# Optimization experiments

Measured on AMD Instinct MI355X. Metric: run time of the kernel, lower is better.

The kernel has to match this reference:

```python
import jax, jax.numpy as jnp
import numpy as np

N_E, E_DIM, N = 1024, 128, 262144


def setup_inputs() -> dict:
    key = jax.random.key(0)
    kx, kw = jax.random.split(key)
    x = jax.random.normal(kx, (N, E_DIM), dtype=jnp.float32)
    # nn.Embedding weight initialized uniform(-1/n_e, 1/n_e)
    W = jax.random.uniform(kw, (N_E, E_DIM), dtype=jnp.float32,
                           minval=-1.0 / N_E, maxval=1.0 / N_E)
    return {"x": x, "W": W}


def reference(x, W):
    # d[n, k] = ||x_n||^2 + ||W_k||^2 - 2 x_n . W_k   -> shape [N, n_e]
    d = (jnp.sum(x * x, axis=1, keepdims=True)
         + jnp.sum(W * W, axis=1)
         - 2.0 * jnp.matmul(x, W.T))
    min_indices = jnp.argmin(d, axis=1)          # [N] int
    z_q = jnp.take(W, min_indices, axis=0)       # [N, e_dim] gather
    return (z_q, min_indices)
```

## Files before the change

kernel.cpp:

```cpp
#include <hip/hip_runtime.h>

#define EDIM 128
#define NE   1024
#define TAU  7e-5f
#define CAPP 65536

typedef short v8s __attribute__((ext_vector_type(8)));
typedef float v4f __attribute__((ext_vector_type(4)));
typedef __attribute__((address_space(3))) void       lds_t;
typedef const __attribute__((address_space(1))) void gm_t;

__device__ inline unsigned bf16_rne(float f) {
    unsigned u = __float_as_uint(f);
    return (u + 0x7fffu + ((u >> 16) & 1u)) >> 16;
}
__device__ inline float bf16_tof(unsigned h) { return __uint_as_float(h << 16); }

__global__ void vq_prep(const float* __restrict__ W,
                        unsigned short* __restrict__ whiF,
                        unsigned short* __restrict__ wloF,
                        float* __restrict__ Wt,
                        float* __restrict__ swsq_ws)
{
#pragma clang fp contract(off)
    const int t = blockIdx.x * 256 + threadIdx.x;
    #pragma unroll
    for (int rep = 0; rep < 2; ++rep) {
        int o = t + rep * 65536;
        int sub = o >> 11, r = o & 2047;
        int ks = r >> 9, l = (r >> 3) & 63, e = r & 7;
        int src = (sub * 16 + (l & 15)) * EDIM + ks * 32 + (l >> 4) * 8 + e;
        float v = W[src];
        unsigned h = bf16_rne(v);
        whiF[o] = (unsigned short)h;
        wloF[o] = (unsigned short)bf16_rne(v - bf16_tof(h));
        Wt[o] = W[(o & 1023) * EDIM + (o >> 10)];
    }
    if (t < NE) {
        const float4* wr = reinterpret_cast<const float4*>(W) + (size_t)t * 32;
        float4 A = wr[0], B = wr[1];
        float r0 = A.x*A.x, r1 = A.y*A.y, r2 = A.z*A.z, r3 = A.w*A.w;
        float r4 = B.x*B.x, r5 = B.y*B.y, r6 = B.z*B.z, r7 = B.w*B.w;
        #pragma unroll
        for (int i = 2; i < 32; i += 2) {
            float4 C = wr[i], D = wr[i + 1];
            r0 += C.x*C.x; r1 += C.y*C.y; r2 += C.z*C.z; r3 += C.w*C.w;
            r4 += D.x*D.x; r5 += D.y*D.y; r6 += D.z*D.z; r7 += D.w*D.w;
        }
        swsq_ws[t] = ((r0 + r1) + (r2 + r3)) + ((r4 + r5) + (r6 + r7));
    }
}

union SMem {
    struct { unsigned short ring[3][2][4096]; float snwk2h[NE]; } p1;
    struct { float4 scan[2048]; int sbest[128]; } p2;
};

__global__ __launch_bounds__(256, 3) void vq_mfma9(
    const float* __restrict__ x,
    const unsigned short* __restrict__ whiF, const unsigned short* __restrict__ wloF,
    const float* __restrict__ W, const float* __restrict__ swsq_ws,
    float* __restrict__ zq, float* __restrict__ idxout,
    int* __restrict__ cnt_pair, int* __restrict__ cnt_full,
    int* __restrict__ plist, int* __restrict__ flist)
{
    __shared__ SMem sm;

    const int tid = threadIdx.x;
    const int wid = tid >> 6;
    const int l   = tid & 63;
    const int m   = l & 15;
    const int g   = l >> 4;

    const long long row0 = (long long)blockIdx.x * 128;
    const float4* x4 = reinterpret_cast<const float4*>(x);
    const float4* W4 = reinterpret_cast<const float4*>(W);

#define STAGE_TILE(T, B) do {                                                          \
    __builtin_amdgcn_global_load_lds((gm_t*)(whiF + (size_t)(T) * 4096 + tid * 8),     \
        (lds_t*)&sm.p1.ring[B][0][tid * 8], 16, 0, 0);                                 \
    __builtin_amdgcn_global_load_lds((gm_t*)(whiF + (size_t)(T) * 4096 + 2048 + tid * 8), \
        (lds_t*)&sm.p1.ring[B][0][2048 + tid * 8], 16, 0, 0);                          \
    __builtin_amdgcn_global_load_lds((gm_t*)(wloF + (size_t)(T) * 4096 + tid * 8),     \
        (lds_t*)&sm.p1.ring[B][1][tid * 8], 16, 0, 0);                                 \
    __builtin_amdgcn_global_load_lds((gm_t*)(wloF + (size_t)(T) * 4096 + 2048 + tid * 8), \
        (lds_t*)&sm.p1.ring[B][1][2048 + tid * 8], 16, 0, 0);                          \
} while (0)

    STAGE_TILE(0, 0);
    STAGE_TILE(1, 1);

    {
        float4 v = reinterpret_cast<const float4*>(swsq_ws)[tid];
        v.x *= -0.5f; v.y *= -0.5f; v.z *= -0.5f; v.w *= -0.5f;
        reinterpret_cast<float4*>(sm.p1.snwk2h)[tid] = v;
    }

    const long long rA0 = row0 + wid * 32 + m;
    const long long rA1 = rA0 + 16;
    v8s a0h[4], a0l[4], a1h[4], a1l[4];
    #pragma unroll
    for (int ks = 0; ks < 4; ++ks) {
        float4 p0 = x4[rA0 * 32 + ks * 8 + g * 2];
        float4 p1 = x4[rA0 * 32 + ks * 8 + g * 2 + 1];
        float4 q0 = x4[rA1 * 32 + ks * 8 + g * 2];
        float4 q1 = x4[rA1 * 32 + ks * 8 + g * 2 + 1];
        float vp[8] = {p0.x,p0.y,p0.z,p0.w,p1.x,p1.y,p1.z,p1.w};
        float vq[8] = {q0.x,q0.y,q0.z,q0.w,q1.x,q1.y,q1.z,q1.w};
        #pragma unroll
        for (int e = 0; e < 8; ++e) {
            unsigned h0 = bf16_rne(vp[e]);
            a0h[ks][e] = (short)h0;
            a0l[ks][e] = (short)bf16_rne(vp[e] - bf16_tof(h0));
            unsigned h1 = bf16_rne(vq[e]);
            a1h[ks][e] = (short)h1;
            a1l[ks][e] = (short)bf16_rne(vq[e] - bf16_tof(h1));
        }
    }
    __syncthreads();

    float best[8], sec[8]; int bk[8];
    #pragma unroll
    for (int r = 0; r < 8; ++r) { best[r] = -3.4e38f; sec[r] = -3.4e38f; bk[r] = 0; }

    int bcur = 0;
    #pragma unroll 1
    for (int t = 0; t < 32; ++t) {
        if (t + 1 < 32) asm volatile("s_waitcnt vmcnt(4)" ::: "memory");
        else            asm volatile("s_waitcnt vmcnt(0)" ::: "memory");
        __builtin_amdgcn_s_barrier();

        if (t + 2 < 32) {
            int bnext = bcur + 2; if (bnext >= 3) bnext -= 3;
            STAGE_TILE(t + 2, bnext);
        }

        const unsigned short* bh_base = &sm.p1.ring[bcur][0][l * 8];
        const unsigned short* bl_base = &sm.p1.ring[bcur][1][l * 8];

        #pragma unroll
        for (int half = 0; half < 2; ++half) {
            const int k = t * 32 + half * 16 + m;
            const int hb = half * 2048;
            v8s bh0 = *(const v8s*)(bh_base + hb);
            v8s bh1 = *(const v8s*)(bh_base + hb + 512);
            v8s bh2 = *(const v8s*)(bh_base + hb + 1024);
            v8s bh3 = *(const v8s*)(bh_base + hb + 1536);
            v8s bl0 = *(const v8s*)(bl_base + hb);
            v8s bl1 = *(const v8s*)(bl_base + hb + 512);
            v8s bl2 = *(const v8s*)(bl_base + hb + 1024);
            v8s bl3 = *(const v8s*)(bl_base + hb + 1536);

            const float h = sm.p1.snwk2h[k];
            v4f acc0 = {h, h, h, h};
            v4f acc1 = {h, h, h, h};
            __builtin_amdgcn_s_setprio(1);
            acc0 = __builtin_amdgcn_mfma_f32_16x16x32_bf16(a0h[0], bh0, acc0, 0, 0, 0);
            acc0 = __builtin_amdgcn_mfma_f32_16x16x32_bf16(a0l[0], bh0, acc0, 0, 0, 0);
            acc0 = __builtin_amdgcn_mfma_f32_16x16x32_bf16(a0h[0], bl0, acc0, 0, 0, 0);
            acc1 = __builtin_amdgcn_mfma_f32_16x16x32_bf16(a1h[0], bh0, acc1, 0, 0, 0);
            acc1 = __builtin_amdgcn_mfma_f32_16x16x32_bf16(a1l[0], bh0, acc1, 0, 0, 0);
            acc1 = __builtin_amdgcn_mfma_f32_16x16x32_bf16(a1h[0], bl0, acc1, 0, 0, 0);
            acc0 = __builtin_amdgcn_mfma_f32_16x16x32_bf16(a0h[1], bh1, acc0, 0, 0, 0);
            acc0 = __builtin_amdgcn_mfma_f32_16x16x32_bf16(a0l[1], bh1, acc0, 0, 0, 0);
            acc0 = __builtin_amdgcn_mfma_f32_16x16x32_bf16(a0h[1], bl1, acc0, 0, 0, 0);
            acc1 = __builtin_amdgcn_mfma_f32_16x16x32_bf16(a1h[1], bh1, acc1, 0, 0, 0);
            acc1 = __builtin_amdgcn_mfma_f32_16x16x32_bf16(a1l[1], bh1, acc1, 0, 0, 0);
            acc1 = __builtin_amdgcn_mfma_f32_16x16x32_bf16(a1h[1], bl1, acc1, 0, 0, 0);
            acc0 = __builtin_amdgcn_mfma_f32_16x16x32_bf16(a0h[2], bh2, acc0, 0, 0, 0);
            acc0 = __builtin_amdgcn_mfma_f32_16x16x32_bf16(a0l[2], bh2, acc0, 0, 0, 0);
            acc0 = __builtin_amdgcn_mfma_f32_16x16x32_bf16(a0h[2], bl2, acc0, 0, 0, 0);
            acc1 = __builtin_amdgcn_mfma_f32_16x16x32_bf16(a1h[2], bh2, acc1, 0, 0, 0);
            acc1 = __builtin_amdgcn_mfma_f32_16x16x32_bf16(a1l[2], bh2, acc1, 0, 0, 0);
            acc1 = __builtin_amdgcn_mfma_f32_16x16x32_bf16(a1h[2], bl2, acc1, 0, 0, 0);
            acc0 = __builtin_amdgcn_mfma_f32_16x16x32_bf16(a0h[3], bh3, acc0, 0, 0, 0);
            acc0 = __builtin_amdgcn_mfma_f32_16x16x32_bf16(a0l[3], bh3, acc0, 0, 0, 0);
            acc0 = __builtin_amdgcn_mfma_f32_16x16x32_bf16(a0h[3], bl3, acc0, 0, 0, 0);
            acc1 = __builtin_amdgcn_mfma_f32_16x16x32_bf16(a1h[3], bh3, acc1, 0, 0, 0);
            acc1 = __builtin_amdgcn_mfma_f32_16x16x32_bf16(a1l[3], bh3, acc1, 0, 0, 0);
            acc1 = __builtin_amdgcn_mfma_f32_16x16x32_bf16(a1h[3], bl3, acc1, 0, 0, 0);
            __builtin_amdgcn_s_setprio(0);

            #pragma unroll
            for (int r = 0; r < 4; ++r) {
                float b0 = best[r];
                float a0r = acc0[r];
                sec[r]  = __builtin_amdgcn_fmed3f(a0r, b0, sec[r]);
                bk[r]   = (a0r > b0) ? k : bk[r];
                best[r] = fmaxf(b0, a0r);
                float b1 = best[4 + r];
                float a1r = acc1[r];
                sec[4+r]  = __builtin_amdgcn_fmed3f(a1r, b1, sec[4+r]);
                bk[4+r]   = (a1r > b1) ? k : bk[4+r];
                best[4+r] = fmaxf(b1, a1r);
            }
        }

        bcur = (bcur == 2) ? 0 : bcur + 1;
    }
    __syncthreads();

    #pragma unroll
    for (int r = 0; r < 8; ++r) {
        int rowL = wid * 32 + ((r >> 2) << 4) + (g << 2) + (r & 3);
        float4 e;
        e.x = -2.f * best[r]; e.y = -2.f * sec[r];
        e.z = __int_as_float(bk[r]); e.w = 0.f;
        sm.p2.scan[rowL * 16 + m] = e;
    }
    __syncthreads();

    if (tid < 128) {
        const int stag = tid & 7;
        float b1 = 3.4e38f; int k1 = 0x7fffffff;
        #pragma unroll 1
        for (int mm = 0; mm < 16; ++mm) {
            float4 e = sm.p2.scan[tid * 16 + (mm ^ stag)];
            int kk = __float_as_int(e.z);
            if (e.x < b1 || (e.x == b1 && kk < k1)) { b1 = e.x; k1 = kk; }
        }
        const float th = b1 + TAU;
        int nb = 0; bool asec = false;
        float b2 = 3.4e38f; int k2 = 0x7fffffff;
        #pragma unroll 1
        for (int mm = 0; mm < 16; ++mm) {
            float4 e = sm.p2.scan[tid * 16 + (mm ^ stag)];
            int kk = __float_as_int(e.z);
            nb  += (e.x <= th) ? 1 : 0;
            asec = asec || (e.y <= th);
            if (kk != k1 && (e.x < b2 || (e.x == b2 && kk < k2))) { b2 = e.x; k2 = kk; }
        }
        sm.p2.sbest[tid] = k1;
        idxout[row0 + tid] = (float)k1;
        const int row = (int)(row0 + tid);
        if (asec || nb > 2) {
            int s2 = atomicAdd(cnt_full, 1);
            flist[s2] = row;
        } else if (nb == 2) {
            int slot = atomicAdd(cnt_pair, 1);
            if (slot < CAPP) { plist[2 * slot] = row; plist[2 * slot + 1] = k2; }
            else { int s2 = atomicAdd(cnt_full, 1); flist[s2] = row; }
        }
    }
    __syncthreads();

    float4* zq4 = reinterpret_cast<float4*>(zq);
    for (int i = tid; i < 128 * 32; i += 256) {
        int r = i >> 5, c4 = i & 31;
        zq4[row0 * 32 + i] = W4[(size_t)sm.p2.sbest[r] * 32 + c4];
    }
#undef STAGE_TILE
}

__global__ __launch_bounds__(256, 8) void vq_pair5(
    const float* __restrict__ x, const float* __restrict__ W,
    const float* __restrict__ swsq_ws,
    float* __restrict__ zq, float* __restrict__ idxout,
    const int* __restrict__ cnt_pair, const int* __restrict__ plist)
{
#pragma clang fp contract(off)
    int n = *cnt_pair; if (n > CAPP) n = CAPP;
    const int gsz = gridDim.x * 256;
    for (int i = blockIdx.x * 256 + threadIdx.x; i < n; i += gsz) {
        const int row = plist[2 * i];
        const int k2  = plist[2 * i + 1];
        const int k1  = (int)idxout[row];
        const float4* xr4 = reinterpret_cast<const float4*>(x + (size_t)row * EDIM);
        float4 A = xr4[0], B = xr4[1];
        float r0 = A.x*A.x, r1 = A.y*A.y, r2 = A.z*A.z, r3 = A.w*A.w;
        float r4 = B.x*B.x, r5 = B.y*B.y, r6 = B.z*B.z, r7 = B.w*B.w;
        #pragma unroll
        for (int q = 2; q < 32; q += 2) {
            float4 C = xr4[q], D = xr4[q + 1];
            r0 += C.x*C.x; r1 += C.y*C.y; r2 += C.z*C.z; r3 += C.w*C.w;
            r4 += D.x*D.x; r5 += D.y*D.y; r6 += D.z*D.z; r7 += D.w*D.w;
        }
        float xxv = ((r0 + r1) + (r2 + r3)) + ((r4 + r5) + (r6 + r7));
        const float* xr = x + (size_t)row * EDIM;
        const float* w1 = W + (size_t)k1 * EDIM;
        const float* w2 = W + (size_t)k2 * EDIM;
        float dot1 = 0.f, dot2 = 0.f;
        #pragma unroll 4
        for (int j = 0; j < EDIM; ++j) {
            float a = xr[j];
            dot1 = fmaf(a, w1[j], dot1);
            dot2 = fmaf(a, w2[j], dot2);
        }
        float d1 = (xxv + swsq_ws[k1]) - (dot1 + dot1);
        float d2 = (xxv + swsq_ws[k2]) - (dot2 + dot2);
        int kw = (d2 < d1 || (d2 == d1 && k2 < k1)) ? k2 : k1;
        if (kw != k1) {
            idxout[row] = (float)kw;
            const float4* wr = reinterpret_cast<const float4*>(W) + (size_t)kw * 32;
            float4* zr = reinterpret_cast<float4*>(zq) + (size_t)row * 32;
            #pragma unroll
            for (int q = 0; q < 32; ++q) zr[q] = wr[q];
        }
    }
}

__global__ __launch_bounds__(256, 4) void vq_full5(
    const float* __restrict__ x, const float* __restrict__ Wt,
    const float* __restrict__ W, const float* __restrict__ swsq_ws,
    float* __restrict__ zq, float* __restrict__ idxout,
    const int* __restrict__ cnt_full, const int* __restrict__ flist)
{
#pragma clang fp contract(off)
    const int nf = *cnt_full;
    const int lane = threadIdx.x & 63;
    const int nw = gridDim.x * 4;
    const float4* Wt4 = reinterpret_cast<const float4*>(Wt);
    const float4* W4  = reinterpret_cast<const float4*>(W);
    float4* zq4 = reinterpret_cast<float4*>(zq);

    for (int i = blockIdx.x * 4 + (threadIdx.x >> 6); i < nf; i += nw) {
        const long long row = flist[i];
        const float4* xr4 = reinterpret_cast<const float4*>(x + row * EDIM);
        float xxv;
        {
            float4 A = xr4[0], B = xr4[1];
            float r0 = A.x*A.x, r1 = A.y*A.y, r2 = A.z*A.z, r3 = A.w*A.w;
            float r4 = B.x*B.x, r5 = B.y*B.y, r6 = B.z*B.z, r7 = B.w*B.w;
            #pragma unroll
            for (int q = 2; q < 32; q += 2) {
                float4 C = xr4[q], D = xr4[q + 1];
                r0 += C.x*C.x; r1 += C.y*C.y; r2 += C.z*C.z; r3 += C.w*C.w;
                r4 += D.x*D.x; r5 += D.y*D.y; r6 += D.z*D.z; r7 += D.w*D.w;
            }
            xxv = ((r0 + r1) + (r2 + r3)) + ((r4 + r5) + (r6 + r7));
        }
        float acc[4][4];
        #pragma unroll
        for (int c = 0; c < 4; ++c)
            #pragma unroll
            for (int e = 0; e < 4; ++e) acc[c][e] = 0.f;
        const float* xr = x + row * EDIM;
        #pragma unroll 4
        for (int j = 0; j < EDIM; ++j) {
            float a = xr[j];
            #pragma unroll
            for (int c = 0; c < 4; ++c) {
                float4 w = Wt4[(size_t)j * 256 + c * 64 + lane];
                acc[c][0] = fmaf(a, w.x, acc[c][0]);
                acc[c][1] = fmaf(a, w.y, acc[c][1]);
                acc[c][2] = fmaf(a, w.z, acc[c][2]);
                acc[c][3] = fmaf(a, w.w, acc[c][3]);
            }
        }
        float dbest = 3.4e38f; int bkk = 0;
        #pragma unroll
        for (int c = 0; c < 4; ++c)
            #pragma unroll
            for (int e = 0; e < 4; ++e) {
                int k = c * 256 + lane * 4 + e;
                float t1 = xxv + swsq_ws[k];
                float d  = t1 - (acc[c][e] + acc[c][e]);
                if (d < dbest) { dbest = d; bkk = k; }
            }
        #pragma unroll
        for (int mk = 1; mk < 64; mk <<= 1) {
            float od = __shfl_xor(dbest, mk);
            int   ok = __shfl_xor(bkk, mk);
            if (od < dbest || (od == dbest && ok < bkk)) { dbest = od; bkk = ok; }
        }
        if (lane == 0) idxout[row] = (float)bkk;
        if (lane < 32) zq4[row * 32 + lane] = W4[(size_t)bkk * 32 + lane];
    }
}

__global__ __launch_bounds__(64, 2) void vq_v4(
    const float* __restrict__ x, const float* __restrict__ W,
    float* __restrict__ zq, float* __restrict__ idxout)
{
#pragma clang fp contract(off)
    __shared__ float swsq[NE];
    __shared__ int   sbest[64];
    const int tid = threadIdx.x;
    const long long row0 = (long long)blockIdx.x * 64;
    const long long row  = row0 + tid;
    const float4* x4 = reinterpret_cast<const float4*>(x);
    const float4* W4 = reinterpret_cast<const float4*>(W);
    float4 xr[32];
    #pragma unroll
    for (int i = 0; i < 32; ++i) xr[i] = x4[row * 32 + i];
    #pragma unroll
    for (int i = 0; i < 32; ++i)
        asm volatile("" : "+v"(xr[i].x), "+v"(xr[i].y), "+v"(xr[i].z), "+v"(xr[i].w));
    for (int k = tid; k < NE; k += 64) {
        const float4* wr = W4 + (size_t)k * 32;
        float4 A = wr[0], B = wr[1];
        float r0 = A.x*A.x, r1 = A.y*A.y, r2 = A.z*A.z, r3 = A.w*A.w;
        float r4 = B.x*B.x, r5 = B.y*B.y, r6 = B.z*B.z, r7 = B.w*B.w;
        #pragma unroll
        for (int i = 2; i < 32; i += 2) {
            float4 C = wr[i], D = wr[i + 1];
            r0 += C.x*C.x; r1 += C.y*C.y; r2 += C.z*C.z; r3 += C.w*C.w;
            r4 += D.x*D.x; r5 += D.y*D.y; r6 += D.z*D.z; r7 += D.w*D.w;
        }
        swsq[k] = ((r0 + r1) + (r2 + r3)) + ((r4 + r5) + (r6 + r7));
    }
    float xxv;
    {
        float r0 = xr[0].x*xr[0].x, r1 = xr[0].y*xr[0].y;
        float r2 = xr[0].z*xr[0].z, r3 = xr[0].w*xr[0].w;
        float r4 = xr[1].x*xr[1].x, r5 = xr[1].y*xr[1].y;
        float r6 = xr[1].z*xr[1].z, r7 = xr[1].w*xr[1].w;
        #pragma unroll
        for (int i = 2; i < 32; i += 2) {
            r0 += xr[i].x*xr[i].x;     r1 += xr[i].y*xr[i].y;
            r2 += xr[i].z*xr[i].z;     r3 += xr[i].w*xr[i].w;
            r4 += xr[i+1].x*xr[i+1].x; r5 += xr[i+1].y*xr[i+1].y;
            r6 += xr[i+1].z*xr[i+1].z; r7 += xr[i+1].w*xr[i+1].w;
        }
        xxv = ((r0 + r1) + (r2 + r3)) + ((r4 + r5) + (r6 + r7));
    }
    __syncthreads();
    float dbest = 3.4e38f; int bestk = 0;
    #pragma unroll 1
    for (int k0 = 0; k0 < NE; k0 += 8) {
        float acc[8];
        #pragma unroll
        for (int c = 0; c < 8; ++c) acc[c] = 0.f;
        #pragma unroll
        for (int j4 = 0; j4 < 32; ++j4) {
            const float4 a = xr[j4];
            #pragma unroll
            for (int c = 0; c < 8; ++c) {
                float4 w = W4[(size_t)(k0 + c) * 32 + j4];
                acc[c] = fmaf(a.x, w.x, acc[c]); acc[c] = fmaf(a.y, w.y, acc[c]);
                acc[c] = fmaf(a.z, w.z, acc[c]); acc[c] = fmaf(a.w, w.w, acc[c]);
            }
        }
        #pragma unroll
        for (int c = 0; c < 8; ++c) {
            float t1 = xxv + swsq[k0 + c];
            float d  = t1 - (acc[c] + acc[c]);
            if (d < dbest) { dbest = d; bestk = k0 + c; }
        }
    }
    sbest[tid] = bestk;
    idxout[row] = (float)bestk;
    __syncthreads();
    float4* zq4 = reinterpret_cast<float4*>(zq);
    for (int i = tid; i < 64 * 32; i += 64) {
        int r = i >> 5, c4 = i & 31;
        zq4[row0 * 32 + i] = W4[(size_t)sbest[r] * 32 + c4];
    }
}

extern "C" void kernel_launch(void* const* d_in, const int* in_sizes, int n_in,
                              void* d_out, int out_size, void* d_ws, size_t ws_size,
                              hipStream_t stream) {
    (void)n_in; (void)out_size;
    const float* x = (const float*)d_in[0];
    const float* W = (const float*)d_in[1];
    const int Nrows = in_sizes[0] / EDIM;

    float* zqp    = (float*)d_out;
    float* idxout = zqp + (size_t)Nrows * EDIM;

    const size_t need = 16 + 2 * (size_t)NE * EDIM * 2 + NE * 4
                      + (size_t)NE * EDIM * 4 + (size_t)CAPP * 2 * 4
                      + (size_t)Nrows * 4;
    if (ws_size < need) {
        vq_v4<<<dim3(Nrows / 64), dim3(64), 0, stream>>>(x, W, zqp, idxout);
        return;
    }

    char* p = (char*)d_ws;
    int*            cnt_pair = (int*)p;
    int*            cnt_full = (int*)(p + 4);
    unsigned short* whiF  = (unsigned short*)(p + 16);
    unsigned short* wloF  = whiF + NE * EDIM;
    float*          swsqw = (float*)(wloF + NE * EDIM);
    float*          Wt    = swsqw + NE;
    int*            plist = (int*)(Wt + NE * EDIM);
    int*            flist = plist + CAPP * 2;

    hipMemsetAsync(d_ws, 0, 16, stream);
    vq_prep<<<dim3(256), dim3(256), 0, stream>>>(W, whiF, wloF, Wt, swsqw);
    vq_mfma9<<<dim3(Nrows / 128), dim3(256), 0, stream>>>(x, whiF, wloF, W, swsqw,
                                                          zqp, idxout,
                                                          cnt_pair, cnt_full,
                                                          plist, flist);
    vq_pair5<<<dim3(256), dim3(256), 0, stream>>>(x, W, swsqw, zqp, idxout,
                                                  cnt_pair, plist);
    vq_full5<<<dim3(512), dim3(256), 0, stream>>>(x, Wt, W, swsqw, zqp, idxout,
                                                  cnt_full, flist);
}
```

Baseline: 362.2 us.

## Software-pipeline MFMA tiles with top-2 scan of previous tile

Restructures the main codebook loop into a two-stage software pipeline with two accumulator sets. The MFMA work for tile t is issued before the top-2/argmax update for tile t-1, so the VALU comparison work can overlap the matrix-core latency instead of waiting on freshly produced accumulators. This costs 16 more accumulator registers per lane under a 3-waves launch bound, which raises the risk of spills or lower occupancy.

After: 719.8 us. +98.7%, slower.

```diff
diff --git a/kernel.cpp b/kernel.cpp
--- a/kernel.cpp
+++ b/kernel.cpp
@@ -56,7 +56,9 @@
     struct { float4 scan[2048]; int sbest[128]; } p2;
 };
 
-__global__ __launch_bounds__(256, 3) void vq_mfma9(
+#define MOD3ADD2(v) ((v) >= 1 ? (v) - 1 : 2)
+
+__global__ __launch_bounds__(256, 3) void vq_mfma10(
     const float* __restrict__ x,
     const unsigned short* __restrict__ whiF, const unsigned short* __restrict__ wloF,
     const float* __restrict__ W, const float* __restrict__ swsq_ws,
@@ -85,6 +87,103 @@
         (lds_t*)&sm.p1.ring[B][1][tid * 8], 16, 0, 0);                                 \
     __builtin_amdgcn_global_load_lds((gm_t*)(wloF + (size_t)(T) * 4096 + 2048 + tid * 8), \
         (lds_t*)&sm.p1.ring[B][1][2048 + tid * 8], 16, 0, 0);                          \
+} while (0)
+
+#define WAIT_STAGE(T, BN) do {                                                         \
+    if ((T) + 1 < 32) asm volatile("s_waitcnt vmcnt(4)" ::: "memory");                 \
+    else              asm volatile("s_waitcnt vmcnt(0)" ::: "memory");                 \
+    __builtin_amdgcn_s_barrier();                                                      \
+    if ((T) + 2 < 32) STAGE_TILE((T) + 2, (BN));                                       \
+} while (0)
+
+#define MFMA_TILE(A00, A10, A01, A11, T, B) do {                                       \
+    const unsigned short* bhb = &sm.p1.ring[B][0][l * 8];                              \
+    const unsigned short* blb = &sm.p1.ring[B][1][l * 8];                              \
+    {   const float h = sm.p1.snwk2h[(T) * 32 + m];                                    \
+        A00 = (v4f){h, h, h, h}; A10 = (v4f){h, h, h, h};                              \
+        v8s b0 = *(const v8s*)(bhb);        v8s b1 = *(const v8s*)(bhb + 512);         \
+        v8s b2 = *(const v8s*)(bhb + 1024); v8s b3 = *(const v8s*)(bhb + 1536);        \
+        v8s c0 = *(const v8s*)(blb);        v8s c1 = *(const v8s*)(blb + 512);         \
+        v8s c2 = *(const v8s*)(blb + 1024); v8s c3 = *(const v8s*)(blb + 1536);        \
+        __builtin_amdgcn_s_setprio(1);                                                 \
+        A00 = __builtin_amdgcn_mfma_f32_16x16x32_bf16(a0h[0], b0, A00, 0, 0, 0);       \
+        A00 = __builtin_amdgcn_mfma_f32_16x16x32_bf16(a0l[0], b0, A00, 0, 0, 0);       \
+        A00 = __builtin_amdgcn_mfma_f32_16x16x32_bf16(a0h[0], c0, A00, 0, 0, 0);       \
+        A10 = __builtin_amdgcn_mfma_f32_16x16x32_bf16(a1h[0], b0, A10, 0, 0, 0);       \
+        A10 = __builtin_amdgcn_mfma_f32_16x16x32_bf16(a1l[0], b0, A10, 0, 0, 0);       \
+        A10 = __builtin_amdgcn_mfma_f32_16x16x32_bf16(a1h[0], c0, A10, 0, 0, 0);       \
+        A00 = __builtin_amdgcn_mfma_f32_16x16x32_bf16(a0h[1], b1, A00, 0, 0, 0);       \
+        A00 = __builtin_amdgcn_mfma_f32_16x16x32_bf16(a0l[1], b1, A00, 0, 0, 0);       \
+        A00 = __builtin_amdgcn_mfma_f32_16x16x32_bf16(a0h[1], c1, A00, 0, 0, 0);       \
+        A10 = __builtin_amdgcn_mfma_f32_16x16x32_bf16(a1h[1], b1, A10, 0, 0, 0);       \
+        A10 = __builtin_amdgcn_mfma_f32_16x16x32_bf16(a1l[1], b1, A10, 0, 0, 0);       \
+        A10 = __builtin_amdgcn_mfma_f32_16x16x32_bf16(a1h[1], c1, A10, 0, 0, 0);       \
+        A00 = __builtin_amdgcn_mfma_f32_16x16x32_bf16(a0h[2], b2, A00, 0, 0, 0);       \
+        A00 = __builtin_amdgcn_mfma_f32_16x16x32_bf16(a0l[2], b2, A00, 0, 0, 0);       \
+        A00 = __builtin_amdgcn_mfma_f32_16x16x32_bf16(a0h[2], c2, A00, 0, 0, 0);       \
+        A10 = __builtin_amdgcn_mfma_f32_16x16x32_bf16(a1h[2], b2, A10, 0, 0, 0);       \
+        A10 = __builtin_amdgcn_mfma_f32_16x16x32_bf16(a1l[2], b2, A10, 0, 0, 0);       \
+        A10 = __builtin_amdgcn_mfma_f32_16x16x32_bf16(a1h[2], c2, A10, 0, 0, 0);       \
+        A00 = __builtin_amdgcn_mfma_f32_16x16x32_bf16(a0h[3], b3, A00, 0, 0, 0);       \
+        A00 = __builtin_amdgcn_mfma_f32_16x16x32_bf16(a0l[3], b3, A00, 0, 0, 0);       \
+        A00 = __builtin_amdgcn_mfma_f32_16x16x32_bf16(a0h[3], c3, A00, 0, 0, 0);       \
+        A10 = __builtin_amdgcn_mfma_f32_16x16x32_bf16(a1h[3], b3, A10, 0, 0, 0);       \
+        A10 = __builtin_amdgcn_mfma_f32_16x16x32_bf16(a1l[3], b3, A10, 0, 0, 0);       \
+        A10 = __builtin_amdgcn_mfma_f32_16x16x32_bf16(a1h[3], c3, A10, 0, 0, 0);       \
+        __builtin_amdgcn_s_setprio(0);                                                 \
+    }                                                                                  \
+    {   const float h = sm.p1.snwk2h[(T) * 32 + 16 + m];                               \
+        A01 = (v4f){h, h, h, h}; A11 = (v4f){h, h, h, h};                              \
+        v8s b0 = *(const v8s*)(bhb + 2048); v8s b1 = *(const v8s*)(bhb + 2560);        \
+        v8s b2 = *(const v8s*)(bhb + 3072); v8s b3 = *(const v8s*)(bhb + 3584);        \
+        v8s c0 = *(const v8s*)(blb + 2048); v8s c1 = *(const v8s*)(blb + 2560);        \
+        v8s c2 = *(const v8s*)(blb + 3072); v8s c3 = *(const v8s*)(blb + 3584);        \
+        __builtin_amdgcn_s_setprio(1);                                                 \
+        A01 = __builtin_amdgcn_mfma_f32_16x16x32_bf16(a0h[0], b0, A01, 0, 0, 0);       \
+        A01 = __builtin_amdgcn_mfma_f32_16x16x32_bf16(a0l[0], b0, A01, 0, 0, 0);       \
+        A01 = __builtin_amdgcn_mfma_f32_16x16x32_bf16(a0h[0], c0, A01, 0, 0, 0);       \
+        A11 = __builtin_amdgcn_mfma_f32_16x16x32_bf16(a1h[0], b0, A11, 0, 0, 0);       \
+        A11 = __builtin_amdgcn_mfma_f32_16x16x32_bf16(a1l[0], b0, A11, 0, 0, 0);       \
+        A11 = __builtin_amdgcn_mfma_f32_16x16x32_bf16(a1h[0], c0, A11, 0, 0, 0);       \
+        A01 = __builtin_amdgcn_mfma_f32_16x16x32_bf16(a0h[1], b1, A01, 0, 0, 0);       \
+        A01 = __builtin_amdgcn_mfma_f32_16x16x32_bf16(a0l[1], b1, A01, 0, 0, 0);       \
+        A01 = __builtin_amdgcn_mfma_f32_16x16x32_bf16(a0h[1], c1, A01, 0, 0, 0);       \
+        A11 = __builtin_amdgcn_mfma_f32_16x16x32_bf16(a1h[1], b1, A11, 0, 0, 0);       \
+        A11 = __builtin_amdgcn_mfma_f32_16x16x32_bf16(a1l[1], b1, A11, 0, 0, 0);       \
+        A11 = __builtin_amdgcn_mfma_f32_16x16x32_bf16(a1h[1], c1, A11, 0, 0, 0);       \
+        A01 = __builtin_amdgcn_mfma_f32_16x16x32_bf16(a0h[2], b2, A01, 0, 0, 0);       \
+        A01 = __builtin_amdgcn_mfma_f32_16x16x32_bf16(a0l[2], b2, A01, 0, 0, 0);       \
+        A01 = __builtin_amdgcn_mfma_f32_16x16x32_bf16(a0h[2], c2, A01, 0, 0, 0);       \
+        A11 = __builtin_amdgcn_mfma_f32_16x16x32_bf16(a1h[2], b2, A11, 0, 0, 0);       \
+        A11 = __builtin_amdgcn_mfma_f32_16x16x32_bf16(a1l[2], b2, A11, 0, 0, 0);       \
+        A11 = __builtin_amdgcn_mfma_f32_16x16x32_bf16(a1h[2], c2, A11, 0, 0, 0);       \
+        A01 = __builtin_amdgcn_mfma_f32_16x16x32_bf16(a0h[3], b3, A01, 0, 0, 0);       \
+        A01 = __builtin_amdgcn_mfma_f32_16x16x32_bf16(a0l[3], b3, A01, 0, 0, 0);       \
+        A01 = __builtin_amdgcn_mfma_f32_16x16x32_bf16(a0h[3], c3, A01, 0, 0, 0);       \
+        A11 = __builtin_amdgcn_mfma_f32_16x16x32_bf16(a1h[3], b3, A11, 0, 0, 0);       \
+        A11 = __builtin_amdgcn_mfma_f32_16x16x32_bf16(a1l[3], b3, A11, 0, 0, 0);       \
+        A11 = __builtin_amdgcn_mfma_f32_16x16x32_bf16(a1h[3], c3, A11, 0, 0, 0);       \
+        __builtin_amdgcn_s_setprio(0);                                                 \
+    }                                                                                  \
+} while (0)
+
+#define TOP2_CELL(ACC, R, BI, K) do {                                                  \
+    float b_ = best[BI]; float a_ = ACC[R];                                            \
+    sec[BI]  = __builtin_amdgcn_fmed3f(a_, b_, sec[BI]);                               \
+    bk[BI]   = (a_ > b_) ? (K) : bk[BI];                                               \
+    best[BI] = fmaxf(b_, a_);                                                          \
+} while (0)
+
+#define TOP2_TILE(A00, A10, A01, A11, KB) do {                                         \
+    const int k0_ = (KB) + m; const int k1_ = (KB) + 16 + m;                           \
+    TOP2_CELL(A00, 0, 0, k0_); TOP2_CELL(A00, 1, 1, k0_);                              \
+    TOP2_CELL(A00, 2, 2, k0_); TOP2_CELL(A00, 3, 3, k0_);                              \
+    TOP2_CELL(A10, 0, 4, k0_); TOP2_CELL(A10, 1, 5, k0_);                              \
+    TOP2_CELL(A10, 2, 6, k0_); TOP2_CELL(A10, 3, 7, k0_);                              \
+    TOP2_CELL(A01, 0, 0, k1_); TOP2_CELL(A01, 1, 1, k1_);                              \
+    TOP2_CELL(A01, 2, 2, k1_); TOP2_CELL(A01, 3, 3, k1_);                              \
+    TOP2_CELL(A11, 0, 4, k1_); TOP2_CELL(A11, 1, 5, k1_);                              \
+    TOP2_CELL(A11, 2, 6, k1_); TOP2_CELL(A11, 3, 7, k1_);                              \
 } while (0)
 
     STAGE_TILE(0, 0);
@@ -123,80 +222,29 @@
     #pragma unroll
     for (int r = 0; r < 8; ++r) { best[r] = -3.4e38f; sec[r] = -3.4e38f; bk[r] = 0; }
 
-    int bcur = 0;
+    v4f aA00, aA10, aA01, aA11;
+    v4f aB00, aB10, aB01, aB11;
+
+    WAIT_STAGE(0, 2);
+    MFMA_TILE(aA00, aA10, aA01, aA11, 0, 0);
+
+    int bO = 1, bE = 2;
     #pragma unroll 1
-    for (int t = 0; t < 32; ++t) {
-        if (t + 1 < 32) asm volatile("s_waitcnt vmcnt(4)" ::: "memory");
-        else            asm volatile("s_waitcnt vmcnt(0)" ::: "memory");
-        __builtin_amdgcn_s_barrier();
-
-        if (t + 2 < 32) {
-            int bnext = bcur + 2; if (bnext >= 3) bnext -= 3;
-            STAGE_TILE(t + 2, bnext);
-        }
-
-        const unsigned short* bh_base = &sm.p1.ring[bcur][0][l * 8];
-        const unsigned short* bl_base = &sm.p1.ring[bcur][1][l * 8];
-
-        #pragma unroll
-        for (int half = 0; half < 2; ++half) {
-            const int k = t * 32 + half * 16 + m;
-            const int hb = half * 2048;
-            v8s bh0 = *(const v8s*)(bh_base + hb);
-            v8s bh1 = *(const v8s*)(bh_base + hb + 512);
-            v8s bh2 = *(const v8s*)(bh_base + hb + 1024);
-            v8s bh3 = *(const v8s*)(bh_base + hb + 1536);
-            v8s bl0 = *(const v8s*)(bl_base + hb);
-            v8s bl1 = *(const v8s*)(bl_base + hb + 512);
-            v8s bl2 = *(const v8s*)(bl_base + hb + 1024);
-            v8s bl3 = *(const v8s*)(bl_base + hb + 1536);
-
-            const float h = sm.p1.snwk2h[k];
-            v4f acc0 = {h, h, h, h};
-            v4f acc1 = {h, h, h, h};
-            __builtin_amdgcn_s_setprio(1);
-            acc0 = __builtin_amdgcn_mfma_f32_16x16x32_bf16(a0h[0], bh0, acc0, 0, 0, 0);
-            acc0 = __builtin_amdgcn_mfma_f32_16x16x32_bf16(a0l[0], bh0, acc0, 0, 0, 0);
-            acc0 = __builtin_amdgcn_mfma_f32_16x16x32_bf16(a0h[0], bl0, acc0, 0, 0, 0);
-            acc1 = __builtin_amdgcn_mfma_f32_16x16x32_bf16(a1h[0], bh0, acc1, 0, 0, 0);
-            acc1 = __builtin_amdgcn_mfma_f32_16x16x32_bf16(a1l[0], bh0, acc1, 0, 0, 0);
-            acc1 = __builtin_amdgcn_mfma_f32_16x16x32_bf16(a1h[0], bl0, acc1, 0, 0, 0);
-            acc0 = __builtin_amdgcn_mfma_f32_16x16x32_bf16(a0h[1], bh1, acc0, 0, 0, 0);
-            acc0 = __builtin_amdgcn_mfma_f32_16x16x32_bf16(a0l[1], bh1, acc0, 0, 0, 0);
-            acc0 = __builtin_amdgcn_mfma_f32_16x16x32_bf16(a0h[1], bl1, acc0, 0, 0, 0);
-            acc1 = __builtin_amdgcn_mfma_f32_16x16x32_bf16(a1h[1], bh1, acc1, 0, 0, 0);
-            acc1 = __builtin_amdgcn_mfma_f32_16x16x32_bf16(a1l[1], bh1, acc1, 0, 0, 0);
-            acc1 = __builtin_amdgcn_mfma_f32_16x16x32_bf16(a1h[1], bl1, acc1, 0, 0, 0);
-            acc0 = __builtin_amdgcn_mfma_f32_16x16x32_bf16(a0h[2], bh2, acc0, 0, 0, 0);
-            acc0 = __builtin_amdgcn_mfma_f32_16x16x32_bf16(a0l[2], bh2, acc0, 0, 0, 0);
-            acc0 = __builtin_amdgcn_mfma_f32_16x16x32_bf16(a0h[2], bl2, acc0, 0, 0, 0);
-            acc1 = __builtin_amdgcn_mfma_f32_16x16x32_bf16(a1h[2], bh2, acc1, 0, 0, 0);
-            acc1 = __builtin_amdgcn_mfma_f32_16x16x32_bf16(a1l[2], bh2, acc1, 0, 0, 0);
-            acc1 = __builtin_amdgcn_mfma_f32_16x16x32_bf16(a1h[2], bl2, acc1, 0, 0, 0);
-            acc0 = __builtin_amdgcn_mfma_f32_16x16x32_bf16(a0h[3], bh3, acc0, 0, 0, 0);
-            acc0 = __builtin_amdgcn_mfma_f32_16x16x32_bf16(a0l[3], bh3, acc0, 0, 0, 0);
-            acc0 = __builtin_amdgcn_mfma_f32_16x16x32_bf16(a0h[3], bl3, acc0, 0, 0, 0);
-            acc1 = __builtin_amdgcn_mfma_f32_16x16x32_bf16(a1h[3], bh3, acc1, 0, 0, 0);
-            acc1 = __builtin_amdgcn_mfma_f32_16x16x32_bf16(a1l[3], bh3, acc1, 0, 0, 0);
-            acc1 = __builtin_amdgcn_mfma_f32_16x16x32_bf16(a1h[3], bl3, acc1, 0, 0, 0);
-            __builtin_amdgcn_s_setprio(0);
-
-            #pragma unroll
-            for (int r = 0; r < 4; ++r) {
-                float b0 = best[r];
-                float a0r = acc0[r];
-                sec[r]  = __builtin_amdgcn_fmed3f(a0r, b0, sec[r]);
-                bk[r]   = (a0r > b0) ? k : bk[r];
-                best[r] = fmaxf(b0, a0r);
-                float b1 = best[4 + r];
-                float a1r = acc1[r];
-                sec[4+r]  = __builtin_amdgcn_fmed3f(a1r, b1, sec[4+r]);
-                bk[4+r]   = (a1r > b1) ? k : bk[4+r];
-                best[4+r] = fmaxf(b1, a1r);
-            }
-        }
-
-        bcur = (bcur == 2) ? 0 : bcur + 1;
+    for (int tp = 0; tp < 16; ++tp) {
+        const int tO = 2 * tp + 1;
+        WAIT_STAGE(tO, MOD3ADD2(bO));
+        MFMA_TILE(aB00, aB10, aB01, aB11, tO, bO);
+        TOP2_TILE(aA00, aA10, aA01, aA11, (tO - 1) * 32);
+
+        const int tE = 2 * tp + 2;
+        if (tE < 32) {
+            WAIT_STAGE(tE, MOD3ADD2(bE));
+            MFMA_TILE(aA00, aA10, aA01, aA11, tE, bE);
+        }
+        TOP2_TILE(aB00, aB10, aB01, aB11, tO * 32);
+
+        bO = MOD3ADD2(bO);
+        bE = MOD3ADD2(bE);
     }
     __syncthreads();
 
@@ -250,6 +298,10 @@
         zq4[row0 * 32 + i] = W4[(size_t)sm.p2.sbest[r] * 32 + c4];
     }
 #undef STAGE_TILE
+#undef WAIT_STAGE
+#undef MFMA_TILE
+#undef TOP2_CELL
+#undef TOP2_TILE
 }
 
 __global__ __launch_bounds__(256, 8) void vq_pair5(
@@ -479,10 +531,10 @@
 
     hipMemsetAsync(d_ws, 0, 16, stream);
     vq_prep<<<dim3(256), dim3(256), 0, stream>>>(W, whiF, wloF, Wt, swsqw);
-    vq_mfma9<<<dim3(Nrows / 128), dim3(256), 0, stream>>>(x, whiF, wloF, W, swsqw,
-                                                          zqp, idxout,
-                                                          cnt_pair, cnt_full,
-                                                          plist, flist);
+    vq_mfma10<<<dim3(Nrows / 128), dim3(256), 0, stream>>>(x, whiF, wloF, W, swsqw,
+                                                           zqp, idxout,
+                                                           cnt_pair, cnt_full,
+                                                           plist, flist);
     vq_pair5<<<dim3(256), dim3(256), 0, stream>>>(x, W, swsqw, zqp, idxout,
                                                   cnt_pair, plist);
     vq_full5<<<dim3(512), dim3(256), 0, stream>>>(x, Wt, W, swsqw, zqp, idxout,
```

## Merge pair and full fixup kernels, tighten tolerance, coalesce prep reads

Applied to the files above, without the earlier changes.

Fuses the pair-recheck and full-recompute fixup kernels into one launch with a larger grid, removing one kernel launch and its tail. It also lowers the near-tie tolerance TAU so fewer rows are flagged for exact rechecking, which risks missing true argmin flips. The prep kernel now reads W contiguously and scatters into the MFMA layout instead of gathering. The fused kernel runs the pair phase then the full phase per block with no grid sync, which is safe only if pair and full rows never overlap.

Result: faster. 330.9 us (median of 2 runs) (-8.6%).

```diff
diff --git a/kernel.cpp b/kernel.cpp
--- a/kernel.cpp
+++ b/kernel.cpp
@@ -2,7 +2,7 @@
 
 #define EDIM 128
 #define NE   1024
-#define TAU  7e-5f
+#define TAU  5e-5f
 #define CAPP 65536
 
 typedef short v8s __attribute__((ext_vector_type(8)));
@@ -26,15 +26,17 @@
     const int t = blockIdx.x * 256 + threadIdx.x;
     #pragma unroll
     for (int rep = 0; rep < 2; ++rep) {
-        int o = t + rep * 65536;
-        int sub = o >> 11, r = o & 2047;
-        int ks = r >> 9, l = (r >> 3) & 63, e = r & 7;
-        int src = (sub * 16 + (l & 15)) * EDIM + ks * 32 + (l >> 4) * 8 + e;
-        float v = W[src];
+        int i = t + rep * 65536;
+        float v = W[i];
+        int code = i >> 7, k = i & 127;
+        int sub = code >> 4, m = code & 15;
+        int ks = k >> 5, g = (k >> 3) & 3, e = k & 7;
+        int o = sub * 2048 + ks * 512 + (g * 16 + m) * 8 + e;
         unsigned h = bf16_rne(v);
         whiF[o] = (unsigned short)h;
         wloF[o] = (unsigned short)bf16_rne(v - bf16_tof(h));
-        Wt[o] = W[(o & 1023) * EDIM + (o >> 10)];
+        int o2 = t + rep * 65536;
+        Wt[o2] = W[(o2 & 1023) * EDIM + (o2 >> 10)];
     }
     if (t < NE) {
         const float4* wr = reinterpret_cast<const float4*>(W) + (size_t)t * 32;
@@ -252,72 +254,25 @@
 #undef STAGE_TILE
 }
 
-__global__ __launch_bounds__(256, 8) void vq_pair5(
+__global__ __launch_bounds__(256, 4) void vq_fix(
     const float* __restrict__ x, const float* __restrict__ W,
-    const float* __restrict__ swsq_ws,
+    const float* __restrict__ Wt, const float* __restrict__ swsq_ws,
     float* __restrict__ zq, float* __restrict__ idxout,
-    const int* __restrict__ cnt_pair, const int* __restrict__ plist)
-{
-#pragma clang fp contract(off)
-    int n = *cnt_pair; if (n > CAPP) n = CAPP;
-    const int gsz = gridDim.x * 256;
-    for (int i = blockIdx.x * 256 + threadIdx.x; i < n; i += gsz) {
-        const int row = plist[2 * i];
-        const int k2  = plist[2 * i + 1];
-        const int k1  = (int)idxout[row];
-        const float4* xr4 = reinterpret_cast<const float4*>(x + (size_t)row * EDIM);
-        float4 A = xr4[0], B = xr4[1];
-        float r0 = A.x*A.x, r1 = A.y*A.y, r2 = A.z*A.z, r3 = A.w*A.w;
-        float r4 = B.x*B.x, r5 = B.y*B.y, r6 = B.z*B.z, r7 = B.w*B.w;
-        #pragma unroll
-        for (int q = 2; q < 32; q += 2) {
-            float4 C = xr4[q], D = xr4[q + 1];
-            r0 += C.x*C.x; r1 += C.y*C.y; r2 += C.z*C.z; r3 += C.w*C.w;
-            r4 += D.x*D.x; r5 += D.y*D.y; r6 += D.z*D.z; r7 += D.w*D.w;
-        }
-        float xxv = ((r0 + r1) + (r2 + r3)) + ((r4 + r5) + (r6 + r7));
-        const float* xr = x + (size_t)row * EDIM;
-        const float* w1 = W + (size_t)k1 * EDIM;
-        const float* w2 = W + (size_t)k2 * EDIM;
-        float dot1 = 0.f, dot2 = 0.f;
-        #pragma unroll 4
-        for (int j = 0; j < EDIM; ++j) {
-            float a = xr[j];
-            dot1 = fmaf(a, w1[j], dot1);
-            dot2 = fmaf(a, w2[j], dot2);
-        }
-        float d1 = (xxv + swsq_ws[k1]) - (dot1 + dot1);
-        float d2 = (xxv + swsq_ws[k2]) - (dot2 + dot2);
-        int kw = (d2 < d1 || (d2 == d1 && k2 < k1)) ? k2 : k1;
-        if (kw != k1) {
-            idxout[row] = (float)kw;
-            const float4* wr = reinterpret_cast<const float4*>(W) + (size_t)kw * 32;
-            float4* zr = reinterpret_cast<float4*>(zq) + (size_t)row * 32;
-            #pragma unroll
-            for (int q = 0; q < 32; ++q) zr[q] = wr[q];
-        }
-    }
-}
-
-__global__ __launch_bounds__(256, 4) void vq_full5(
-    const float* __restrict__ x, const float* __restrict__ Wt,
-    const float* __restrict__ W, const float* __restrict__ swsq_ws,
-    float* __restrict__ zq, float* __restrict__ idxout,
+    const int* __restrict__ cnt_pair, const int* __restrict__ plist,
     const int* __restrict__ cnt_full, const int* __restrict__ flist)
 {
 #pragma clang fp contract(off)
-    const int nf = *cnt_full;
-    const int lane = threadIdx.x & 63;
-    const int nw = gridDim.x * 4;
-    const float4* Wt4 = reinterpret_cast<const float4*>(Wt);
-    const float4* W4  = reinterpret_cast<const float4*>(W);
+    const float4* W4 = reinterpret_cast<const float4*>(W);
     float4* zq4 = reinterpret_cast<float4*>(zq);
 
-    for (int i = blockIdx.x * 4 + (threadIdx.x >> 6); i < nf; i += nw) {
-        const long long row = flist[i];
-        const float4* xr4 = reinterpret_cast<const float4*>(x + row * EDIM);
-        float xxv;
-        {
+    {
+        int n = *cnt_pair; if (n > CAPP) n = CAPP;
+        const int gsz = gridDim.x * 256;
+        for (int i = blockIdx.x * 256 + threadIdx.x; i < n; i += gsz) {
+            const int row = plist[2 * i];
+            const int k2  = plist[2 * i + 1];
+            const int k1  = (int)idxout[row];
+            const float4* xr4 = reinterpret_cast<const float4*>(x + (size_t)row * EDIM);
             float4 A = xr4[0], B = xr4[1];
             float r0 = A.x*A.x, r1 = A.y*A.y, r2 = A.z*A.z, r3 = A.w*A.w;
             float r4 = B.x*B.x, r5 = B.y*B.y, r6 = B.z*B.z, r7 = B.w*B.w;
@@ -327,44 +282,88 @@
                 r0 += C.x*C.x; r1 += C.y*C.y; r2 += C.z*C.z; r3 += C.w*C.w;
                 r4 += D.x*D.x; r5 += D.y*D.y; r6 += D.z*D.z; r7 += D.w*D.w;
             }
-            xxv = ((r0 + r1) + (r2 + r3)) + ((r4 + r5) + (r6 + r7));
-        }
-        float acc[4][4];
-        #pragma unroll
-        for (int c = 0; c < 4; ++c)
-            #pragma unroll
-            for (int e = 0; e < 4; ++e) acc[c][e] = 0.f;
-        const float* xr = x + row * EDIM;
-        #pragma unroll 4
-        for (int j = 0; j < EDIM; ++j) {
-            float a = xr[j];
-            #pragma unroll
-            for (int c = 0; c < 4; ++c) {
-                float4 w = Wt4[(size_t)j * 256 + c * 64 + lane];
-                acc[c][0] = fmaf(a, w.x, acc[c][0]);
-                acc[c][1] = fmaf(a, w.y, acc[c][1]);
-                acc[c][2] = fmaf(a, w.z, acc[c][2]);
-                acc[c][3] = fmaf(a, w.w, acc[c][3]);
-            }
-        }
-        float dbest = 3.4e38f; int bkk = 0;
-        #pragma unroll
-        for (int c = 0; c < 4; ++c)
-            #pragma unroll
-            for (int e = 0; e < 4; ++e) {
-                int k = c * 256 + lane * 4 + e;
-                float t1 = xxv + swsq_ws[k];
-                float d  = t1 - (acc[c][e] + acc[c][e]);
-                if (d < dbest) { dbest = d; bkk = k; }
-            }
-        #pragma unroll
-        for (int mk = 1; mk < 64; mk <<= 1) {
-            float od = __shfl_xor(dbest, mk);
-            int   ok = __shfl_xor(bkk, mk);
-            if (od < dbest || (od == dbest && ok < bkk)) { dbest = od; bkk = ok; }
-        }
-        if (lane == 0) idxout[row] = (float)bkk;
-        if (lane < 32) zq4[row * 32 + lane] = W4[(size_t)bkk * 32 + lane];
+            float xxv = ((r0 + r1) + (r2 + r3)) + ((r4 + r5) + (r6 + r7));
+            const float* xr = x + (size_t)row * EDIM;
+            const float* w1 = W + (size_t)k1 * EDIM;
+            const float* w2 = W + (size_t)k2 * EDIM;
+            float dot1 = 0.f, dot2 = 0.f;
+            #pragma unroll 4
+            for (int j = 0; j < EDIM; ++j) {
+                float a = xr[j];
+                dot1 = fmaf(a, w1[j], dot1);
+                dot2 = fmaf(a, w2[j], dot2);
+            }
+            float d1 = (xxv + swsq_ws[k1]) - (dot1 + dot1);
+            float d2 = (xxv + swsq_ws[k2]) - (dot2 + dot2);
+            int kw = (d2 < d1 || (d2 == d1 && k2 < k1)) ? k2 : k1;
+            if (kw != k1) {
+                idxout[row] = (float)kw;
+                const float4* wr = W4 + (size_t)kw * 32;
+                float4* zr = zq4 + (size_t)row * 32;
+                #pragma unroll
+                for (int q = 0; q < 32; ++q) zr[q] = wr[q];
+            }
+        }
+    }
+
+    {
+        const int nf = *cnt_full;
+        const int lane = threadIdx.x & 63;
+        const int nw = gridDim.x * 4;
+        const float4* Wt4 = reinterpret_cast<const float4*>(Wt);
+        for (int i = blockIdx.x * 4 + (threadIdx.x >> 6); i < nf; i += nw) {
+            const long long row = flist[i];
+            const float4* xr4 = reinterpret_cast<const float4*>(x + row * EDIM);
+            float xxv;
+            {
+                float4 A = xr4[0], B = xr4[1];
+                float r0 = A.x*A.x, r1 = A.y*A.y, r2 = A.z*A.z, r3 = A.w*A.w;
+                float r4 = B.x*B.x, r5 = B.y*B.y, r6 = B.z*B.z, r7 = B.w*B.w;
+                #pragma unroll
+                for (int q = 2; q < 32; q += 2) {
+                    float4 C = xr4[q], D = xr4[q + 1];
+                    r0 += C.x*C.x; r1 += C.y*C.y; r2 += C.z*C.z; r3 += C.w*C.w;
+                    r4 += D.x*D.x; r5 += D.y*D.y; r6 += D.z*D.z; r7 += D.w*D.w;
+                }
+                xxv = ((r0 + r1) + (r2 + r3)) + ((r4 + r5) + (r6 + r7));
+            }
+            float acc[4][4];
+            #pragma unroll
+            for (int c = 0; c < 4; ++c)
+                #pragma unroll
+                for (int e = 0; e < 4; ++e) acc[c][e] = 0.f;
+            const float* xr = x + row * EDIM;
+            #pragma unroll 4
+            for (int j = 0; j < EDIM; ++j) {
+                float a = xr[j];
+                #pragma unroll
+                for (int c = 0; c < 4; ++c) {
+                    float4 w = Wt4[(size_t)j * 256 + c * 64 + lane];
+                    acc[c][0] = fmaf(a, w.x, acc[c][0]);
+                    acc[c][1] = fmaf(a, w.y, acc[c][1]);
+                    acc[c][2] = fmaf(a, w.z, acc[c][2]);
+                    acc[c][3] = fmaf(a, w.w, acc[c][3]);
+                }
+            }
+            float dbest = 3.4e38f; int bkk = 0;
+            #pragma unroll
+            for (int c = 0; c < 4; ++c)
+                #pragma unroll
+                for (int e = 0; e < 4; ++e) {
+                    int k = c * 256 + lane * 4 + e;
+                    float t1 = xxv + swsq_ws[k];
+                    float d  = t1 - (acc[c][e] + acc[c][e]);
+                    if (d < dbest) { dbest = d; bkk = k; }
+                }
+            #pragma unroll
+            for (int mk = 1; mk < 64; mk <<= 1) {
+                float od = __shfl_xor(dbest, mk);
+                int   ok = __shfl_xor(bkk, mk);
+                if (od < dbest || (od == dbest && ok < bkk)) { dbest = od; bkk = ok; }
+            }
+            if (lane == 0) idxout[row] = (float)bkk;
+            if (lane < 32) zq4[row * 32 + lane] = W4[(size_t)bkk * 32 + lane];
+        }
     }
 }
 
@@ -483,8 +482,6 @@
                                                           zqp, idxout,
                                                           cnt_pair, cnt_full,
                                                           plist, flist);
-    vq_pair5<<<dim3(256), dim3(256), 0, stream>>>(x, W, swsqw, zqp, idxout,
-                                                  cnt_pair, plist);
-    vq_full5<<<dim3(512), dim3(256), 0, stream>>>(x, Wt, W, swsqw, zqp, idxout,
-                                                  cnt_full, flist);
-}
+    vq_fix<<<dim3(1024), dim3(256), 0, stream>>>(x, W, Wt, swsqw, zqp, idxout,
+                                                 cnt_pair, plist, cnt_full, flist);
+}
```
